# Kernel tuning notes

Hardware: AMD Instinct MI355X
Metric: run time of the kernel (lower is better)

Reference implementation:

```python
import jax, jax.numpy as jnp
import numpy as np

H = 4  # heads_n (sequential refinement heads)


def _layer_norm(x, g, b, eps=1e-5):
    mu = jnp.mean(x, axis=-1, keepdims=True)
    var = jnp.mean((x - mu) ** 2, axis=-1, keepdims=True)
    return (x - mu) * jax.lax.rsqrt(var + eps) * g + b


def _pose_enc(S, F):
    # Faithful translation of PoseEncoding._make_pe_buffer
    pos = jnp.arange(S, dtype=jnp.float32)[:, None]            # (S,1)
    div = (1.0 / (1000.0 ** (2.0 * jnp.arange(F, dtype=jnp.float32) / F)))[None, :]  # (1,F)
    pe = jnp.zeros((S, F), jnp.float32)
    pe = pe.at[0::2, :].set(jnp.sin(pos[0::2] * div))
    pe = pe.at[1::2, :].set(jnp.cos(pos[1::2] * div))
    return pe  # (S,F)


def setup_inputs() -> dict:
    key = jax.random.key(0)
    ks = jax.random.split(key, 6)
    B, S, C = 4, 2048, 1024
    std = 0.02
    return {
        "x": jax.random.normal(ks[0], (B, S, C), jnp.float32),
        "fc_in_w": jax.random.normal(ks[1], (C, C), jnp.float32) * std,
        "fc_in_b": jnp.zeros((C,), jnp.float32),
        "ln_g": jnp.ones((C,), jnp.float32),
        "ln_b": jnp.zeros((C,), jnp.float32),
        "qkv_w": jax.random.normal(ks[2], (H, 3 * C, C), jnp.float32) * std,
        "qkv_b": jnp.zeros((H, 3 * C), jnp.float32),
        "proj_w": jax.random.normal(ks[3], (H, C, C), jnp.float32) * std,
        "proj_b": jnp.zeros((H, C), jnp.float32),
        "fc_out_w": jax.random.normal(ks[4], (C, C), jnp.float32) * std,
        "fc_out_b": jnp.zeros((C,), jnp.float32),
    }


def reference(x, fc_in_w, fc_in_b, ln_g, ln_b, qkv_w, qkv_b, proj_w, proj_b, fc_out_w, fc_out_b):
    B, S, C = x.shape
    gelu = lambda t: jax.nn.gelu(t, approximate=False)  # nn.GELU default = exact erf
    h = x @ fc_in_w.T + fc_in_b                         # fc_in
    h = _layer_norm(h, ln_g, ln_b)
    pred = None
    for i in range(qkv_w.shape[0]):                     # sequential heads loop (eval mode: dropout = identity)
        qkv = gelu(h @ qkv_w[i].T + qkv_b[i])           # (B,S,3C)
        qkv = qkv.reshape(B, S, 3, C)
        q, k, v = qkv[:, :, 0], qkv[:, :, 1], qkv[:, :, 2]
        scores = jnp.einsum('bsc,btc->bst', q, k) * (1.0 / C)  # (B,S,S), mask is None
        att = jnp.einsum('bst,btc->bsc', scores, v)     # matmul BEFORE softmax (non-standard order)
        att = jax.nn.softmax(att, axis=-1)
        h = gelu(att @ proj_w[i].T + proj_b[i])
        if pred is None:
            pred = h
        else:
            h = h + pred                                 # residual with first head's output
    out = h @ fc_out_w.T + fc_out_b
    return out + _pose_enc(S, out.shape[-1])[None]      # PoseEncoding add
```

## Files before the change

### kernel.cpp

```cpp
#include <hip/hip_runtime.h>
#include <math.h>

typedef unsigned short u16;
typedef __bf16 bf16x8 __attribute__((ext_vector_type(8)));
typedef float f32x4  __attribute__((ext_vector_type(4)));
typedef float f32x16 __attribute__((ext_vector_type(16)));
typedef u16   u16x4  __attribute__((ext_vector_type(4)));
typedef u16   u16x8  __attribute__((ext_vector_type(8)));

#define GPTR(p) ((__attribute__((address_space(1))) void*)(p))
#define LPTR(p) ((__attribute__((address_space(3))) void*)(p))

__device__ __forceinline__ float bf2f(u16 h) { return __uint_as_float(((unsigned)h) << 16); }
__device__ __forceinline__ u16 f2bf(float f) {
    unsigned u = __float_as_uint(f);
    return (u16)((u + 0x7fffu + ((u >> 16) & 1u)) >> 16);
}
__device__ __forceinline__ float gelu_f(float x) {
    float u = 0.7978845608f * x * (1.0f + 0.044715f * x * x);
    float e = __expf(2.0f * u);
    float t = 1.0f - 2.0f / (e + 1.0f);
    return 0.5f * x * (1.0f + t);
}

template<int MODE>
__global__ __launch_bounds__(256, 3)
void gemm_g(const u16* __restrict__ A, int lda, long sA,
            const u16* __restrict__ B, long sB,
            void* __restrict__ Cout, int ldc, long sC,
            const float* __restrict__ bias,
            const u16* __restrict__ addend,
            u16* __restrict__ kgr, u16* __restrict__ vgr,
            int K, float scale)
{
    __shared__ u16 lds[16384];
    u16* lA = lds;
    const int t    = threadIdx.x;
    const int lane = t & 63;
    const int wid  = t >> 6;
    const int wm   = (wid & 1) * 64;
    const int wn   = (wid >> 1) * 64;
    const int m32  = lane & 31;
    const int h    = lane >> 5;
    const int bz   = blockIdx.z;

    const long rowA0 = (long)blockIdx.y * 128;
    const long colB0 = (long)blockIdx.x * 128;
    const u16* Ab = A + (long)bz * sA + rowA0 * lda;

    const int rt  = t >> 3;
    const int kcg = ((t & 7) ^ (rt & 7)) * 8;
    const u16* gA[4];
    #pragma unroll
    for (int j = 0; j < 4; j++) gA[j] = Ab + (long)(j * 32 + rt) * lda + kcg;
    u16* dA = lA + t * 8;

    const int nt0 = (int)((colB0 + wn) >> 5);
    const long ktn = (long)(K >> 4) * 512;
    const u16* gb0 = B + (long)bz * sB + (long)nt0 * ktn + lane * 8;
    const u16* gb1 = gb0 + ktn;

    f32x16 acc[2][2];
    #pragma unroll
    for (int i = 0; i < 2; i++)
        #pragma unroll
        for (int j = 0; j < 2; j++)
            #pragma unroll
            for (int r = 0; r < 16; r++) acc[i][j][r] = 0.f;

    const int sg = m32 & 7;
    const u16* fA[4];
    #pragma unroll
    for (int kh = 0; kh < 4; kh++)
        fA[kh] = lA + (wm + m32) * 64 + 8 * ((kh * 2 + h) ^ sg);

    #pragma unroll
    for (int j = 0; j < 4; j++)
        __builtin_amdgcn_global_load_lds(GPTR(gA[j]), LPTR(dA + j * 2048), 16, 0, 0);
    bf16x8 bc[2][4], bn[2][4];
    #pragma unroll
    for (int kh = 0; kh < 4; kh++) {
        bc[0][kh] = *(const bf16x8*)(gb0 + kh * 512);
        bc[1][kh] = *(const bf16x8*)(gb1 + kh * 512);
    }

    const int niter = K >> 6;
    for (int it = 0; it < niter; ++it) {
        __syncthreads();
        const int kn = (it + 1) << 6;
        if (kn < K) {
            const int nb = (it + 1) & 1;
            #pragma unroll
            for (int j = 0; j < 4; j++)
                __builtin_amdgcn_global_load_lds(GPTR(gA[j] + kn),
                                                 LPTR(dA + nb * 8192 + j * 2048), 16, 0, 0);
            #pragma unroll
            for (int kh = 0; kh < 4; kh++) {
                bn[0][kh] = *(const bf16x8*)(gb0 + (long)kn * 32 + kh * 512);
                bn[1][kh] = *(const bf16x8*)(gb1 + (long)kn * 32 + kh * 512);
            }
        }
        const int cbo = (it & 1) * 8192;
        #pragma unroll
        for (int kh = 0; kh < 4; kh++) {
            bf16x8 a0 = *(const bf16x8*)(fA[kh] + cbo);
            bf16x8 a1 = *(const bf16x8*)(fA[kh] + cbo + 2048);
            acc[0][0] = __builtin_amdgcn_mfma_f32_32x32x16_bf16(a0, bc[0][kh], acc[0][0], 0, 0, 0);
            acc[0][1] = __builtin_amdgcn_mfma_f32_32x32x16_bf16(a0, bc[1][kh], acc[0][1], 0, 0, 0);
            acc[1][0] = __builtin_amdgcn_mfma_f32_32x32x16_bf16(a1, bc[0][kh], acc[1][0], 0, 0, 0);
            acc[1][1] = __builtin_amdgcn_mfma_f32_32x32x16_bf16(a1, bc[1][kh], acc[1][1], 0, 0, 0);
        }
        #pragma unroll
        for (int kh = 0; kh < 4; kh++) { bc[0][kh] = bn[0][kh]; bc[1][kh] = bn[1][kh]; }
    }

    float* Cf = (float*)Cout + (long)bz * sC;
    u16*   Cu = (u16*)Cout + (long)bz * sC;
    float* sw_ = (float*)lds + wid * 1024;
    const long rb = rowA0 + wm;
    const long cb = colB0 + wn;
    const int prow = lane >> 3;
    const int c4   = (lane & 7) * 4;
    #pragma unroll
    for (int mi = 0; mi < 2; mi++) {
        #pragma unroll
        for (int ni = 0; ni < 2; ni++) {
            const int colg = (int)(cb + ni * 32 + m32);
            float bv = 0.0f;
            if constexpr (MODE >= 2) bv = bias[colg];
            #pragma unroll
            for (int r = 0; r < 16; r++) {
                float v = acc[mi][ni][r];
                if constexpr (MODE == 1) v *= scale;
                v += bv;
                if constexpr (MODE == 3 || MODE == 4 || MODE == 6) v = gelu_f(v);
                const int rowfn = (r & 3) + 8 * (r >> 2) + 4 * h;
                sw_[rowfn * 32 + (m32 ^ ((rowfn & 3) * 8))] = v;
            }
            const int seg = (MODE == 6) ? (int)(colB0 >> 10) : 0;
            if (MODE != 6 || seg == 0) {
                #pragma unroll
                for (int p = 0; p < 4; p++) {
                    const int  row  = p * 8 + prow;
                    const long grow = rb + mi * 32 + row;
                    const long gcol = cb + ni * 32 + c4;
                    const int  key  = (row & 3) * 8;
                    f32x4 v = *(const f32x4*)&sw_[row * 32 + (c4 ^ key)];
                    if constexpr (MODE == 4) {
                        u16x4 ad = *(const u16x4*)&addend[grow * (long)ldc + gcol];
                        #pragma unroll
                        for (int e = 0; e < 4; e++) v[e] += bf2f(ad[e]);
                    }
                    if constexpr (MODE == 5) {
                        *(f32x4*)&Cf[grow * (long)ldc + gcol] = v;
                    } else {
                        u16x4 o = { f2bf(v[0]), f2bf(v[1]), f2bf(v[2]), f2bf(v[3]) };
                        *(u16x4*)&Cu[grow * (long)ldc + gcol] = o;
                    }
                }
            } else if (seg == 1) {
                const int b   = (int)(rb >> 11);
                const int nt  = ((int)(rb & 2047) + mi * 32) >> 5;
                const int kt0 = ((int)cb + ni * 32 - 1024) >> 4;
                u16* base = kgr + (long)b * 2097152 + ((long)(nt * 64 + kt0) * 64 + lane) * 8;
                #pragma unroll
                for (int q2 = 0; q2 < 2; q2++) {
                    const int g0  = q2 * 16 + h * 8;
                    const int key = (m32 & 3) * 8;
                    f32x4 u0 = *(const f32x4*)&sw_[m32 * 32 + (g0 ^ key)];
                    f32x4 u1 = *(const f32x4*)&sw_[m32 * 32 + (g0 ^ key) + 4];
                    u16x8 o = { f2bf(u0[0]), f2bf(u0[1]), f2bf(u0[2]), f2bf(u0[3]),
                                f2bf(u1[0]), f2bf(u1[1]), f2bf(u1[2]), f2bf(u1[3]) };
                    *(u16x8*)(base + q2 * 512) = o;
                }
            } else {
                const int b   = (int)(rb >> 11);
                const int kt0 = ((int)(rb & 2047) + mi * 32) >> 4;
                const int nt  = ((int)cb + ni * 32 - 2048) >> 5;
                u16* base = vgr + (long)b * 2097152 + ((long)(nt * 128 + kt0) * 64 + lane) * 8;
                #pragma unroll
                for (int q2 = 0; q2 < 2; q2++) {
                    float vv[8];
                    #pragma unroll
                    for (int j = 0; j < 8; j++) {
                        const int r = q2 * 16 + h * 8 + j;
                        vv[j] = sw_[r * 32 + (m32 ^ ((r & 3) * 8))];
                    }
                    u16x8 o = { f2bf(vv[0]), f2bf(vv[1]), f2bf(vv[2]), f2bf(vv[3]),
                                f2bf(vv[4]), f2bf(vv[5]), f2bf(vv[6]), f2bf(vv[7]) };
                    *(u16x8*)(base + q2 * 512) = o;
                }
            }
        }
    }
}

__global__ __launch_bounds__(256)
void cvt_x(const float* __restrict__ in, u16* __restrict__ out, long n)
{
    long i = ((long)blockIdx.x * 256 + threadIdx.x) * 4;
    if (i < n) {
        float4 v = *(const float4*)(in + i);
        u16x4 o = { f2bf(v.x), f2bf(v.y), f2bf(v.z), f2bf(v.w) };
        *(u16x4*)(out + i) = o;
    }
}

__global__ __launch_bounds__(256)
void cvt_wg(const float* __restrict__ qkvw, u16* __restrict__ dqkv,
            const float* __restrict__ projw, u16* __restrict__ dproj,
            const float* __restrict__ fciw, u16* __restrict__ dfci,
            const float* __restrict__ fcow, u16* __restrict__ dfco)
{
    __shared__ u16 sl[2048];
    const int nt = blockIdx.y;
    const int ks = blockIdx.x;
    const int t  = threadIdx.x;
    const float* src; u16* dst; int nl;
    if      (nt < 384) { src = qkvw;  dst = dqkv;  nl = nt; }
    else if (nt < 512) { src = projw; dst = dproj; nl = nt - 384; }
    else if (nt < 544) { src = fciw;  dst = dfci;  nl = nt - 512; }
    else               { src = fcow;  dst = dfco;  nl = nt - 544; }
    const int n32 = t >> 3;
    const int kq  = t & 7;
    const float* s = src + ((long)nl * 32 + n32) * 1024 + ks * 64 + kq * 8;
    float4 v0 = *(const float4*)s;
    float4 v1 = *(const float4*)(s + 4);
    u16x8 o = { f2bf(v0.x), f2bf(v0.y), f2bf(v0.z), f2bf(v0.w),
                f2bf(v1.x), f2bf(v1.y), f2bf(v1.z), f2bf(v1.w) };
    const int slot = (kq >> 1) * 64 + (kq & 1) * 32 + n32;
    *(u16x8*)&sl[slot * 8] = o;
    __syncthreads();
    u16* d = dst + (long)nl * 32768 + ks * 2048 + t * 8;
    *(u16x8*)d = *(const u16x8*)&sl[t * 8];
}

__global__ __launch_bounds__(256)
void ln_kernel(const u16* __restrict__ in, u16* __restrict__ out,
               const float* __restrict__ g, const float* __restrict__ b)
{
    const int row = blockIdx.x;
    const int t = threadIdx.x;
    const u16* r = in + (long)row * 1024;
    float x[4];
    float s = 0.f, s2 = 0.f;
    #pragma unroll
    for (int j = 0; j < 4; j++) { x[j] = bf2f(r[t + 256 * j]); s += x[j]; s2 += x[j] * x[j]; }
    __shared__ float sm[8];
    const int lane = t & 63, wid = t >> 6;
    #pragma unroll
    for (int o = 32; o > 0; o >>= 1) { s += __shfl_down(s, o, 64); s2 += __shfl_down(s2, o, 64); }
    if (lane == 0) { sm[wid] = s; sm[4 + wid] = s2; }
    __syncthreads();
    s  = sm[0] + sm[1] + sm[2] + sm[3];
    s2 = sm[4] + sm[5] + sm[6] + sm[7];
    const float mean = s * (1.f / 1024.f);
    const float var  = s2 * (1.f / 1024.f) - mean * mean;
    const float rstd = rsqrtf(var + 1e-5f);
    u16* o = out + (long)row * 1024;
    #pragma unroll
    for (int j = 0; j < 4; j++) {
        int c = t + 256 * j;
        o[c] = f2bf((x[j] - mean) * rstd * g[c] + b[c]);
    }
}

__global__ __launch_bounds__(256)
void softmax_kernel(u16* __restrict__ io)
{
    const int row = blockIdx.x;
    const int t = threadIdx.x;
    u16* r = io + (long)row * 1024;
    float x[4];
    float m = -1e30f;
    #pragma unroll
    for (int j = 0; j < 4; j++) { x[j] = bf2f(r[t + 256 * j]); m = fmaxf(m, x[j]); }
    __shared__ float sm[8];
    const int lane = t & 63, wid = t >> 6;
    #pragma unroll
    for (int o = 32; o > 0; o >>= 1) m = fmaxf(m, __shfl_down(m, o, 64));
    if (lane == 0) sm[wid] = m;
    __syncthreads();
    m = fmaxf(fmaxf(sm[0], sm[1]), fmaxf(sm[2], sm[3]));
    float e[4];
    float s = 0.f;
    #pragma unroll
    for (int j = 0; j < 4; j++) { e[j] = __expf(x[j] - m); s += e[j]; }
    #pragma unroll
    for (int o = 32; o > 0; o >>= 1) s += __shfl_down(s, o, 64);
    if (lane == 0) sm[4 + wid] = s;
    __syncthreads();
    s = sm[4] + sm[5] + sm[6] + sm[7];
    const float inv = 1.f / s;
    #pragma unroll
    for (int j = 0; j < 4; j++) r[t + 256 * j] = f2bf(e[j] * inv);
}

__global__ __launch_bounds__(256)
void add_pe(float* __restrict__ out)
{
    long i = (long)blockIdx.x * 256 + threadIdx.x;
    const int f = (int)(i & 1023);
    const int s = (int)((i >> 10) & 2047);
    const float div = __expf(-(float)f * 0.013491709529261986f);
    const float arg = (float)s * div;
    const float pe = (s & 1) ? cosf(arg) : sinf(arg);
    out[i] += pe;
}

extern "C" void kernel_launch(void* const* d_in, const int* in_sizes, int n_in,
                              void* d_out, int out_size, void* d_ws, size_t ws_size,
                              hipStream_t stream)
{
    const float* x        = (const float*)d_in[0];
    const float* fc_in_w  = (const float*)d_in[1];
    const float* fc_in_b  = (const float*)d_in[2];
    const float* ln_g     = (const float*)d_in[3];
    const float* ln_b     = (const float*)d_in[4];
    const float* qkv_w    = (const float*)d_in[5];
    const float* qkv_b    = (const float*)d_in[6];
    const float* proj_w   = (const float*)d_in[7];
    const float* proj_b   = (const float*)d_in[8];
    const float* fc_out_w = (const float*)d_in[9];
    const float* fc_out_b = (const float*)d_in[10];

    char* w = (char*)d_ws;
    size_t off = 0;
    auto carve = [&](size_t bytes) -> void* {
        void* p = w + off;
        off += (bytes + 255) & ~(size_t)255;
        return p;
    };
    u16* xb   = (u16*)carve(16777216);
    u16* hY   = xb;
    u16* wfci = (u16*)carve(2097152);
    u16* wqkv = (u16*)carve(25165824);
    u16* wprj = (u16*)carve(8388608);
    u16* wfco = (u16*)carve(2097152);
    u16* qb   = (u16*)carve(16777216);
    u16* kgr  = (u16*)carve(16777216);
    u16* vgr  = (u16*)carve(16777216);
    u16* att  = (u16*)carve(16777216);
    u16* hX   = (u16*)carve(16777216);
    u16* pred = (u16*)carve(16777216);
    u16* sc   = (u16*)carve(33554432);

    cvt_x<<<dim3(8192), dim3(256), 0, stream>>>(x, xb, 8388608L);
    cvt_wg<<<dim3(16, 576), dim3(256), 0, stream>>>(qkv_w, wqkv, proj_w, wprj,
                                                    fc_in_w, wfci, fc_out_w, wfco);

    gemm_g<2><<<dim3(8, 64, 1), 256, 0, stream>>>(xb, 1024, 0, wfci, 0,
        qb, 1024, 0, fc_in_b, nullptr, nullptr, nullptr, 1024, 1.0f);
    ln_kernel<<<8192, 256, 0, stream>>>(qb, hX, ln_g, ln_b);

    const u16* hin[4] = { hX, pred, hX, hY };
    u16* hout[4]      = { pred, hX, hY, hX };

    for (int i = 0; i < 4; i++) {
        gemm_g<6><<<dim3(24, 64, 1), 256, 0, stream>>>(hin[i], 1024, 0,
            wqkv + (long)i * 3145728, 0, qb, 1024, 0,
            qkv_b + (long)i * 3072, nullptr, kgr, vgr, 1024, 1.0f);
        gemm_g<1><<<dim3(16, 16, 4), 256, 0, stream>>>(qb, 1024, 2097152,
            kgr, 2097152, sc, 2048, 4194304,
            nullptr, nullptr, nullptr, nullptr, 1024, 1.0f / 1024.0f);
        gemm_g<0><<<dim3(8, 16, 4), 256, 0, stream>>>(sc, 2048, 4194304,
            vgr, 2097152, att, 1024, 2097152,
            nullptr, nullptr, nullptr, nullptr, 2048, 1.0f);
        softmax_kernel<<<8192, 256, 0, stream>>>(att);
        if (i == 0)
            gemm_g<3><<<dim3(8, 64, 1), 256, 0, stream>>>(att, 1024, 0,
                wprj, 0, hout[0], 1024, 0, proj_b, nullptr, nullptr, nullptr, 1024, 1.0f);
        else
            gemm_g<4><<<dim3(8, 64, 1), 256, 0, stream>>>(att, 1024, 0,
                wprj + (long)i * 1048576, 0, hout[i], 1024, 0,
                proj_b + (long)i * 1024, pred, nullptr, nullptr, 1024, 1.0f);
    }

    gemm_g<5><<<dim3(8, 64, 1), 256, 0, stream>>>(hX, 1024, 0, wfco, 0,
        d_out, 1024, 0, fc_out_b, nullptr, nullptr, nullptr, 1024, 1.0f);
    add_pe<<<32768, 256, 0, stream>>>((float*)d_out);
}
```

Before: 1.045 ms.

## Store all GEMM operands in MFMA-fragment layout and drop LDS staging

Every GEMM operand, including the A side, is now stored in a pre-tiled 32x16 MFMA fragment layout. Each wave then loads its fragments straight from global memory into registers, and the LDS double-buffered global_load_lds path for A goes away. LayerNorm, softmax, the score GEMM and the proj GEMMs write their outputs in this tiled layout, which needs an extra attention buffer and a larger score buffer. The x conversion is merged into the weight-conversion kernel. The risks are that there is no software prefetch across k-iterations anymore, so load latency is exposed, and that A tiles are not shared through LDS, so each wave fetches its own fragments.

```diff
diff --git a/kernel.cpp b/kernel.cpp
--- a/kernel.cpp
+++ b/kernel.cpp
@@ -8,9 +8,6 @@
 typedef u16   u16x4  __attribute__((ext_vector_type(4)));
 typedef u16   u16x8  __attribute__((ext_vector_type(8)));
 
-#define GPTR(p) ((__attribute__((address_space(1))) void*)(p))
-#define LPTR(p) ((__attribute__((address_space(3))) void*)(p))
-
 __device__ __forceinline__ float bf2f(u16 h) { return __uint_as_float(((unsigned)h) << 16); }
 __device__ __forceinline__ u16 f2bf(float f) {
     unsigned u = __float_as_uint(f);
@@ -25,16 +22,15 @@
 
 template<int MODE>
 __global__ __launch_bounds__(256, 3)
-void gemm_g(const u16* __restrict__ A, int lda, long sA,
+void gemm_r(const u16* __restrict__ A, long sA,
             const u16* __restrict__ B, long sB,
             void* __restrict__ Cout, int ldc, long sC,
             const float* __restrict__ bias,
             const u16* __restrict__ addend,
-            u16* __restrict__ kgr, u16* __restrict__ vgr,
-            int K, float scale)
-{
-    __shared__ u16 lds[16384];
-    u16* lA = lds;
+            u16* __restrict__ g1, u16* __restrict__ g2,
+            int K, int Kout, float scale)
+{
+    __shared__ float sw[4096];
     const int t    = threadIdx.x;
     const int lane = t & 63;
     const int wid  = t >> 6;
@@ -46,18 +42,11 @@
 
     const long rowA0 = (long)blockIdx.y * 128;
     const long colB0 = (long)blockIdx.x * 128;
-    const u16* Ab = A + (long)bz * sA + rowA0 * lda;
-
-    const int rt  = t >> 3;
-    const int kcg = ((t & 7) ^ (rt & 7)) * 8;
-    const u16* gA[4];
-    #pragma unroll
-    for (int j = 0; j < 4; j++) gA[j] = Ab + (long)(j * 32 + rt) * lda + kcg;
-    u16* dA = lA + t * 8;
-
-    const int nt0 = (int)((colB0 + wn) >> 5);
-    const long ktn = (long)(K >> 4) * 512;
-    const u16* gb0 = B + (long)bz * sB + (long)nt0 * ktn + lane * 8;
+    const long ktn  = (long)(K >> 4) * 512;
+
+    const u16* ga0 = A + (long)bz * sA + ((rowA0 + wm) >> 5) * ktn + lane * 8;
+    const u16* ga1 = ga0 + ktn;
+    const u16* gb0 = B + (long)bz * sB + ((colB0 + wn) >> 5) * ktn + lane * 8;
     const u16* gb1 = gb0 + ktn;
 
     f32x16 acc[2][2];
@@ -68,59 +57,34 @@
             #pragma unroll
             for (int r = 0; r < 16; r++) acc[i][j][r] = 0.f;
 
-    const int sg = m32 & 7;
-    const u16* fA[4];
-    #pragma unroll
-    for (int kh = 0; kh < 4; kh++)
-        fA[kh] = lA + (wm + m32) * 64 + 8 * ((kh * 2 + h) ^ sg);
-
-    #pragma unroll
-    for (int j = 0; j < 4; j++)
-        __builtin_amdgcn_global_load_lds(GPTR(gA[j]), LPTR(dA + j * 2048), 16, 0, 0);
-    bf16x8 bc[2][4], bn[2][4];
-    #pragma unroll
-    for (int kh = 0; kh < 4; kh++) {
-        bc[0][kh] = *(const bf16x8*)(gb0 + kh * 512);
-        bc[1][kh] = *(const bf16x8*)(gb1 + kh * 512);
-    }
-
-    const int niter = K >> 6;
-    for (int it = 0; it < niter; ++it) {
-        __syncthreads();
-        const int kn = (it + 1) << 6;
-        if (kn < K) {
-            const int nb = (it + 1) & 1;
-            #pragma unroll
-            for (int j = 0; j < 4; j++)
-                __builtin_amdgcn_global_load_lds(GPTR(gA[j] + kn),
-                                                 LPTR(dA + nb * 8192 + j * 2048), 16, 0, 0);
-            #pragma unroll
-            for (int kh = 0; kh < 4; kh++) {
-                bn[0][kh] = *(const bf16x8*)(gb0 + (long)kn * 32 + kh * 512);
-                bn[1][kh] = *(const bf16x8*)(gb1 + (long)kn * 32 + kh * 512);
-            }
-        }
-        const int cbo = (it & 1) * 8192;
+    const int ktotal = K >> 4;
+    for (int kt = 0; kt < ktotal; kt += 4) {
+        const long o = (long)kt * 512;
+        bf16x8 a0[4], a1[4], b0[4], b1[4];
         #pragma unroll
-        for (int kh = 0; kh < 4; kh++) {
-            bf16x8 a0 = *(const bf16x8*)(fA[kh] + cbo);
-            bf16x8 a1 = *(const bf16x8*)(fA[kh] + cbo + 2048);
-            acc[0][0] = __builtin_amdgcn_mfma_f32_32x32x16_bf16(a0, bc[0][kh], acc[0][0], 0, 0, 0);
-            acc[0][1] = __builtin_amdgcn_mfma_f32_32x32x16_bf16(a0, bc[1][kh], acc[0][1], 0, 0, 0);
-            acc[1][0] = __builtin_amdgcn_mfma_f32_32x32x16_bf16(a1, bc[0][kh], acc[1][0], 0, 0, 0);
-            acc[1][1] = __builtin_amdgcn_mfma_f32_32x32x16_bf16(a1, bc[1][kh], acc[1][1], 0, 0, 0);
+        for (int j = 0; j < 4; j++) {
+            a0[j] = *(const bf16x8*)(ga0 + o + j * 512);
+            a1[j] = *(const bf16x8*)(ga1 + o + j * 512);
+            b0[j] = *(const bf16x8*)(gb0 + o + j * 512);
+            b1[j] = *(const bf16x8*)(gb1 + o + j * 512);
         }
         #pragma unroll
-        for (int kh = 0; kh < 4; kh++) { bc[0][kh] = bn[0][kh]; bc[1][kh] = bn[1][kh]; }
+        for (int j = 0; j < 4; j++) {
+            acc[0][0] = __builtin_amdgcn_mfma_f32_32x32x16_bf16(a0[j], b0[j], acc[0][0], 0, 0, 0);
+            acc[0][1] = __builtin_amdgcn_mfma_f32_32x32x16_bf16(a0[j], b1[j], acc[0][1], 0, 0, 0);
+            acc[1][0] = __builtin_amdgcn_mfma_f32_32x32x16_bf16(a1[j], b0[j], acc[1][0], 0, 0, 0);
+            acc[1][1] = __builtin_amdgcn_mfma_f32_32x32x16_bf16(a1[j], b1[j], acc[1][1], 0, 0, 0);
+        }
     }
 
     float* Cf = (float*)Cout + (long)bz * sC;
     u16*   Cu = (u16*)Cout + (long)bz * sC;
-    float* sw_ = (float*)lds + wid * 1024;
+    float* sw_ = sw + wid * 1024;
     const long rb = rowA0 + wm;
     const long cb = colB0 + wn;
     const int prow = lane >> 3;
     const int c4   = (lane & 7) * 4;
+    const int key  = (m32 & 3) * 8;
     #pragma unroll
     for (int mi = 0; mi < 2; mi++) {
         #pragma unroll
@@ -137,20 +101,14 @@
                 const int rowfn = (r & 3) + 8 * (r >> 2) + 4 * h;
                 sw_[rowfn * 32 + (m32 ^ ((rowfn & 3) * 8))] = v;
             }
-            const int seg = (MODE == 6) ? (int)(colB0 >> 10) : 0;
-            if (MODE != 6 || seg == 0) {
+            if constexpr (MODE == 0 || MODE == 2 || MODE == 5) {
                 #pragma unroll
                 for (int p = 0; p < 4; p++) {
                     const int  row  = p * 8 + prow;
                     const long grow = rb + mi * 32 + row;
                     const long gcol = cb + ni * 32 + c4;
-                    const int  key  = (row & 3) * 8;
-                    f32x4 v = *(const f32x4*)&sw_[row * 32 + (c4 ^ key)];
-                    if constexpr (MODE == 4) {
-                        u16x4 ad = *(const u16x4*)&addend[grow * (long)ldc + gcol];
-                        #pragma unroll
-                        for (int e = 0; e < 4; e++) v[e] += bf2f(ad[e]);
-                    }
+                    const int  k2   = (row & 3) * 8;
+                    f32x4 v = *(const f32x4*)&sw_[row * 32 + (c4 ^ k2)];
                     if constexpr (MODE == 5) {
                         *(f32x4*)&Cf[grow * (long)ldc + gcol] = v;
                     } else {
@@ -158,37 +116,60 @@
                         *(u16x4*)&Cu[grow * (long)ldc + gcol] = o;
                     }
                 }
-            } else if (seg == 1) {
-                const int b   = (int)(rb >> 11);
-                const int nt  = ((int)(rb & 2047) + mi * 32) >> 5;
-                const int kt0 = ((int)cb + ni * 32 - 1024) >> 4;
-                u16* base = kgr + (long)b * 2097152 + ((long)(nt * 64 + kt0) * 64 + lane) * 8;
+            } else if constexpr (MODE == 1 || MODE == 3 || MODE == 4) {
+                const int mt  = (int)((rb + mi * 32) >> 5);
+                const int kt0 = (int)((cb + ni * 32) >> 4);
+                const long go = (long)bz * sC + ((long)(mt * (Kout >> 4) + kt0)) * 512 + lane * 8;
+                u16* dst = g1 + go;
                 #pragma unroll
                 for (int q2 = 0; q2 < 2; q2++) {
-                    const int g0  = q2 * 16 + h * 8;
-                    const int key = (m32 & 3) * 8;
+                    const int g0 = q2 * 16 + h * 8;
                     f32x4 u0 = *(const f32x4*)&sw_[m32 * 32 + (g0 ^ key)];
                     f32x4 u1 = *(const f32x4*)&sw_[m32 * 32 + (g0 ^ key) + 4];
-                    u16x8 o = { f2bf(u0[0]), f2bf(u0[1]), f2bf(u0[2]), f2bf(u0[3]),
-                                f2bf(u1[0]), f2bf(u1[1]), f2bf(u1[2]), f2bf(u1[3]) };
-                    *(u16x8*)(base + q2 * 512) = o;
-                }
-            } else {
-                const int b   = (int)(rb >> 11);
-                const int kt0 = ((int)(rb & 2047) + mi * 32) >> 4;
-                const int nt  = ((int)cb + ni * 32 - 2048) >> 5;
-                u16* base = vgr + (long)b * 2097152 + ((long)(nt * 128 + kt0) * 64 + lane) * 8;
-                #pragma unroll
-                for (int q2 = 0; q2 < 2; q2++) {
-                    float vv[8];
-                    #pragma unroll
-                    for (int j = 0; j < 8; j++) {
-                        const int r = q2 * 16 + h * 8 + j;
-                        vv[j] = sw_[r * 32 + (m32 ^ ((r & 3) * 8))];
+                    float vv[8] = { u0[0], u0[1], u0[2], u0[3], u1[0], u1[1], u1[2], u1[3] };
+                    if constexpr (MODE == 4) {
+                        u16x8 ad = *(const u16x8*)(addend + go + q2 * 512);
+                        #pragma unroll
+                        for (int e = 0; e < 8; e++) vv[e] += bf2f(ad[e]);
                     }
                     u16x8 o = { f2bf(vv[0]), f2bf(vv[1]), f2bf(vv[2]), f2bf(vv[3]),
                                 f2bf(vv[4]), f2bf(vv[5]), f2bf(vv[6]), f2bf(vv[7]) };
-                    *(u16x8*)(base + q2 * 512) = o;
+                    *(u16x8*)(dst + q2 * 512) = o;
+                }
+            } else {
+                const int seg = (int)(colB0 >> 10);
+                const int b   = (int)(rb >> 11);
+                const int rowb = (int)(rb & 2047) + mi * 32;
+                if (seg < 2) {
+                    const int mt  = rowb >> 5;
+                    const int kt0 = ((int)cb + ni * 32 - seg * 1024) >> 4;
+                    u16* dst = (seg == 0 ? (u16*)Cout : g1)
+                             + (long)b * 2097152 + ((long)(mt * 64 + kt0)) * 512 + lane * 8;
+                    #pragma unroll
+                    for (int q2 = 0; q2 < 2; q2++) {
+                        const int g0 = q2 * 16 + h * 8;
+                        f32x4 u0 = *(const f32x4*)&sw_[m32 * 32 + (g0 ^ key)];
+                        f32x4 u1 = *(const f32x4*)&sw_[m32 * 32 + (g0 ^ key) + 4];
+                        u16x8 o = { f2bf(u0[0]), f2bf(u0[1]), f2bf(u0[2]), f2bf(u0[3]),
+                                    f2bf(u1[0]), f2bf(u1[1]), f2bf(u1[2]), f2bf(u1[3]) };
+                        *(u16x8*)(dst + q2 * 512) = o;
+                    }
+                } else {
+                    const int kt0 = rowb >> 4;
+                    const int nt  = ((int)cb + ni * 32 - 2048) >> 5;
+                    u16* dst = g2 + (long)b * 2097152 + ((long)(nt * 128 + kt0)) * 512 + lane * 8;
+                    #pragma unroll
+                    for (int q2 = 0; q2 < 2; q2++) {
+                        float vv[8];
+                        #pragma unroll
+                        for (int j = 0; j < 8; j++) {
+                            const int r = q2 * 16 + h * 8 + j;
+                            vv[j] = sw_[r * 32 + (m32 ^ ((r & 3) * 8))];
+                        }
+                        u16x8 o = { f2bf(vv[0]), f2bf(vv[1]), f2bf(vv[2]), f2bf(vv[3]),
+                                    f2bf(vv[4]), f2bf(vv[5]), f2bf(vv[6]), f2bf(vv[7]) };
+                        *(u16x8*)(dst + q2 * 512) = o;
+                    }
                 }
             }
         }
@@ -196,31 +177,22 @@
 }
 
 __global__ __launch_bounds__(256)
-void cvt_x(const float* __restrict__ in, u16* __restrict__ out, long n)
-{
-    long i = ((long)blockIdx.x * 256 + threadIdx.x) * 4;
-    if (i < n) {
-        float4 v = *(const float4*)(in + i);
-        u16x4 o = { f2bf(v.x), f2bf(v.y), f2bf(v.z), f2bf(v.w) };
-        *(u16x4*)(out + i) = o;
-    }
-}
-
-__global__ __launch_bounds__(256)
-void cvt_wg(const float* __restrict__ qkvw, u16* __restrict__ dqkv,
-            const float* __restrict__ projw, u16* __restrict__ dproj,
-            const float* __restrict__ fciw, u16* __restrict__ dfci,
-            const float* __restrict__ fcow, u16* __restrict__ dfco)
+void cvt_a(const float* __restrict__ xs, u16* __restrict__ dx,
+           const float* __restrict__ qkvw, u16* __restrict__ dqkv,
+           const float* __restrict__ projw, u16* __restrict__ dproj,
+           const float* __restrict__ fciw, u16* __restrict__ dfci,
+           const float* __restrict__ fcow, u16* __restrict__ dfco)
 {
     __shared__ u16 sl[2048];
     const int nt = blockIdx.y;
     const int ks = blockIdx.x;
     const int t  = threadIdx.x;
     const float* src; u16* dst; int nl;
-    if      (nt < 384) { src = qkvw;  dst = dqkv;  nl = nt; }
-    else if (nt < 512) { src = projw; dst = dproj; nl = nt - 384; }
-    else if (nt < 544) { src = fciw;  dst = dfci;  nl = nt - 512; }
-    else               { src = fcow;  dst = dfco;  nl = nt - 544; }
+    if      (nt < 256) { src = xs;    dst = dx;    nl = nt; }
+    else if (nt < 640) { src = qkvw;  dst = dqkv;  nl = nt - 256; }
+    else if (nt < 768) { src = projw; dst = dproj; nl = nt - 640; }
+    else if (nt < 800) { src = fciw;  dst = dfci;  nl = nt - 768; }
+    else               { src = fcow;  dst = dfco;  nl = nt - 800; }
     const int n32 = t >> 3;
     const int kq  = t & 7;
     const float* s = src + ((long)nl * 32 + n32) * 1024 + ks * 64 + kq * 8;
@@ -235,17 +207,23 @@
     *(u16x8*)d = *(const u16x8*)&sl[t * 8];
 }
 
+__device__ __forceinline__ long gr_off(int r, int k0) {
+    return (long)(r >> 5) * 32768 + (k0 >> 4) * 512
+         + (((k0 >> 3) & 1) * 32 + (r & 31)) * 8 + (k0 & 7);
+}
+
 __global__ __launch_bounds__(256)
 void ln_kernel(const u16* __restrict__ in, u16* __restrict__ out,
                const float* __restrict__ g, const float* __restrict__ b)
 {
     const int row = blockIdx.x;
     const int t = threadIdx.x;
-    const u16* r = in + (long)row * 1024;
+    const int k0 = t * 4;
+    u16x4 xv = *(const u16x4*)&in[(long)row * 1024 + k0];
     float x[4];
     float s = 0.f, s2 = 0.f;
     #pragma unroll
-    for (int j = 0; j < 4; j++) { x[j] = bf2f(r[t + 256 * j]); s += x[j]; s2 += x[j] * x[j]; }
+    for (int j = 0; j < 4; j++) { x[j] = bf2f(xv[j]); s += x[j]; s2 += x[j] * x[j]; }
     __shared__ float sm[8];
     const int lane = t & 63, wid = t >> 6;
     #pragma unroll
@@ -257,24 +235,24 @@
     const float mean = s * (1.f / 1024.f);
     const float var  = s2 * (1.f / 1024.f) - mean * mean;
     const float rstd = rsqrtf(var + 1e-5f);
-    u16* o = out + (long)row * 1024;
-    #pragma unroll
-    for (int j = 0; j < 4; j++) {
-        int c = t + 256 * j;
-        o[c] = f2bf((x[j] - mean) * rstd * g[c] + b[c]);
-    }
+    u16x4 o4;
+    #pragma unroll
+    for (int j = 0; j < 4; j++)
+        o4[j] = f2bf((x[j] - mean) * rstd * g[k0 + j] + b[k0 + j]);
+    *(u16x4*)&out[gr_off(row, k0)] = o4;
 }
 
 __global__ __launch_bounds__(256)
-void softmax_kernel(u16* __restrict__ io)
+void softmax_kernel(const u16* __restrict__ in, u16* __restrict__ out)
 {
     const int row = blockIdx.x;
     const int t = threadIdx.x;
-    u16* r = io + (long)row * 1024;
+    const int k0 = t * 4;
+    u16x4 xv = *(const u16x4*)&in[(long)row * 1024 + k0];
     float x[4];
     float m = -1e30f;
     #pragma unroll
-    for (int j = 0; j < 4; j++) { x[j] = bf2f(r[t + 256 * j]); m = fmaxf(m, x[j]); }
+    for (int j = 0; j < 4; j++) { x[j] = bf2f(xv[j]); m = fmaxf(m, x[j]); }
     __shared__ float sm[8];
     const int lane = t & 63, wid = t >> 6;
     #pragma unroll
@@ -292,8 +270,10 @@
     __syncthreads();
     s = sm[4] + sm[5] + sm[6] + sm[7];
     const float inv = 1.f / s;
-    #pragma unroll
-    for (int j = 0; j < 4; j++) r[t + 256 * j] = f2bf(e[j] * inv);
+    u16x4 o4;
+    #pragma unroll
+    for (int j = 0; j < 4; j++) o4[j] = f2bf(e[j] * inv);
+    *(u16x4*)&out[gr_off(row, k0)] = o4;
 }
 
 __global__ __launch_bounds__(256)
@@ -341,42 +321,44 @@
     u16* kgr  = (u16*)carve(16777216);
     u16* vgr  = (u16*)carve(16777216);
     u16* att  = (u16*)carve(16777216);
+    u16* attg = (u16*)carve(16777216);
     u16* hX   = (u16*)carve(16777216);
     u16* pred = (u16*)carve(16777216);
-    u16* sc   = (u16*)carve(33554432);
-
-    cvt_x<<<dim3(8192), dim3(256), 0, stream>>>(x, xb, 8388608L);
-    cvt_wg<<<dim3(16, 576), dim3(256), 0, stream>>>(qkv_w, wqkv, proj_w, wprj,
-                                                    fc_in_w, wfci, fc_out_w, wfco);
-
-    gemm_g<2><<<dim3(8, 64, 1), 256, 0, stream>>>(xb, 1024, 0, wfci, 0,
-        qb, 1024, 0, fc_in_b, nullptr, nullptr, nullptr, 1024, 1.0f);
-    ln_kernel<<<8192, 256, 0, stream>>>(qb, hX, ln_g, ln_b);
+    u16* sc   = (u16*)carve(67108864);
+
+    cvt_a<<<dim3(16, 832), dim3(256), 0, stream>>>(
+        x, xb, qkv_w, wqkv, proj_w, wprj, fc_in_w, wfci, fc_out_w, wfco);
+
+    gemm_r<2><<<dim3(8, 64, 1), 256, 0, stream>>>(xb, 0, wfci, 0,
+        att, 1024, 0, fc_in_b, nullptr, nullptr, nullptr, 1024, 0, 1.0f);
+    ln_kernel<<<8192, 256, 0, stream>>>(att, hX, ln_g, ln_b);
 
     const u16* hin[4] = { hX, pred, hX, hY };
     u16* hout[4]      = { pred, hX, hY, hX };
 
     for (int i = 0; i < 4; i++) {
-        gemm_g<6><<<dim3(24, 64, 1), 256, 0, stream>>>(hin[i], 1024, 0,
-            wqkv + (long)i * 3145728, 0, qb, 1024, 0,
-            qkv_b + (long)i * 3072, nullptr, kgr, vgr, 1024, 1.0f);
-        gemm_g<1><<<dim3(16, 16, 4), 256, 0, stream>>>(qb, 1024, 2097152,
-            kgr, 2097152, sc, 2048, 4194304,
-            nullptr, nullptr, nullptr, nullptr, 1024, 1.0f / 1024.0f);
-        gemm_g<0><<<dim3(8, 16, 4), 256, 0, stream>>>(sc, 2048, 4194304,
+        gemm_r<6><<<dim3(24, 64, 1), 256, 0, stream>>>(hin[i], 0,
+            wqkv + (long)i * 3145728, 0, qb, 0, 0,
+            qkv_b + (long)i * 3072, nullptr, kgr, vgr, 1024, 0, 1.0f);
+        gemm_r<1><<<dim3(16, 16, 4), 256, 0, stream>>>(qb, 2097152,
+            kgr, 2097152, nullptr, 0, 4194304,
+            nullptr, nullptr, sc, nullptr, 1024, 2048, 1.0f / 1024.0f);
+        gemm_r<0><<<dim3(8, 16, 4), 256, 0, stream>>>(sc, 4194304,
             vgr, 2097152, att, 1024, 2097152,
-            nullptr, nullptr, nullptr, nullptr, 2048, 1.0f);
-        softmax_kernel<<<8192, 256, 0, stream>>>(att);
+            nullptr, nullptr, nullptr, nullptr, 2048, 0, 1.0f);
+        softmax_kernel<<<8192, 256, 0, stream>>>(att, attg);
         if (i == 0)
-            gemm_g<3><<<dim3(8, 64, 1), 256, 0, stream>>>(att, 1024, 0,
-                wprj, 0, hout[0], 1024, 0, proj_b, nullptr, nullptr, nullptr, 1024, 1.0f);
+            gemm_r<3><<<dim3(8, 64, 1), 256, 0, stream>>>(attg, 0,
+                wprj, 0, nullptr, 0, 0, proj_b, nullptr, hout[0], nullptr,
+                1024, 1024, 1.0f);
         else
-            gemm_g<4><<<dim3(8, 64, 1), 256, 0, stream>>>(att, 1024, 0,
-                wprj + (long)i * 1048576, 0, hout[i], 1024, 0,
-                proj_b + (long)i * 1024, pred, nullptr, nullptr, 1024, 1.0f);
+            gemm_r<4><<<dim3(8, 64, 1), 256, 0, stream>>>(attg, 0,
+                wprj + (long)i * 1048576, 0, nullptr, 0, 0,
+                proj_b + (long)i * 1024, pred, hout[i], nullptr,
+                1024, 1024, 1.0f);
     }
 
-    gemm_g<5><<<dim3(8, 64, 1), 256, 0, stream>>>(hX, 1024, 0, wfco, 0,
-        d_out, 1024, 0, fc_out_b, nullptr, nullptr, nullptr, 1024, 1.0f);
+    gemm_r<5><<<dim3(8, 64, 1), 256, 0, stream>>>(hX, 0, wfco, 0,
+        d_out, 1024, 0, fc_out_b, nullptr, nullptr, nullptr, 1024, 0, 1.0f);
     add_pe<<<32768, 256, 0, stream>>>((float*)d_out);
 }
```

Result: slower. 1.097 ms (+4.9%).
